# Performance work log

Measured on AMD Instinct MI355X. Metric: run time of the kernel, lower is better.

The kernel has to match this reference:

```python
import jax, jax.numpy as jnp
import numpy as np

HEADS = 8
D = 1024


def setup_inputs() -> dict:
    key = jax.random.key(0)
    ks = jax.random.split(key, 10)
    B, Sq, Sk = 8, 2048, 2048
    x = jax.random.normal(ks[0], (B, Sq, D), dtype=jnp.float32)
    context = jax.random.normal(ks[1], (B, Sk, D), dtype=jnp.float32)
    # Dense params (glorot-ish scale)
    def dense(k, fin, fout):
        return jax.random.normal(k, (fin, fout), dtype=jnp.float32) / np.sqrt(fin)
    Wq = dense(ks[2], D, HEADS); bq = jnp.zeros((HEADS,), jnp.float32)
    Wk = dense(ks[3], D, HEADS); bk = jnp.zeros((HEADS,), jnp.float32)
    Wv = dense(ks[4], D, HEADS); bv = jnp.zeros((HEADS,), jnp.float32)
    Wo = dense(ks[5], HEADS, D); bo = jnp.zeros((D,), jnp.float32)
    return {"x": x, "context": context, "Wq": Wq, "bq": bq,
            "Wk": Wk, "bk": bk, "Wv": Wv, "bv": bv, "Wo": Wo, "bo": bo}


def reference(x, context, Wq, bq, Wk, bk, Wv, bv, Wo, bo):
    # q: [B,Sq,H], k/v: [B,Sk,H]  (H = heads = projection width, no head split)
    q = jnp.einsum('bsd,dh->bsh', x, Wq) + bq
    k = jnp.einsum('btd,dh->bth', context, Wk) + bk
    v = jnp.einsum('btd,dh->bth', context, Wv) + bv
    # Dot(axes=-1): scores[b,s,t] = q[b,s,:] . k[b,t,:]  -> [B,Sq,Sk]
    scores = jnp.einsum('bsh,bth->bst', q, k)
    weights = jax.nn.softmax(scores, axis=-1)  # no 1/sqrt(d) scaling in original
    # Dot(axes=(-1,1)): out[b,s,h] = sum_t weights[b,s,t] * v[b,t,h]
    out = jnp.einsum('bst,bth->bsh', weights, v)
    return jnp.einsum('bsh,hd->bsd', out, Wo) + bo
```

## Files before the change

kernel.cpp:

```cpp
#include <hip/hip_runtime.h>

constexpr int D = 1024;
constexpr int H = 8;
constexpr int S = 2048;
constexpr int B = 8;
constexpr int NROW = B * S;

__global__ __launch_bounds__(256)
void proj_kernel(const float* __restrict__ x, const float* __restrict__ ctx,
                 const float* __restrict__ Wq, const float* __restrict__ bq,
                 const float* __restrict__ Wk, const float* __restrict__ bk,
                 const float* __restrict__ Wv, const float* __restrict__ bv,
                 float* __restrict__ qo, float* __restrict__ ko,
                 float* __restrict__ vo)
{
    __shared__ float4 xt[32 * 64];
    __shared__ float  red[4 * 64 * 8];

    const int tid   = threadIdx.x;
    const int lane  = tid & 63;
    const int wid_v = tid >> 6;
    const int wid   = __builtin_amdgcn_readfirstlane(wid_v);

    const int bid = (int)blockIdx.x;
    const int tensor = (bid >> 3) % 3;
    const int blk    = (bid / 24) * 8 + (bid & 7);

    const float* W    = (tensor == 0) ? Wq : (tensor == 1) ? Wk : Wv;
    const float* bias = (tensor == 0) ? bq : (tensor == 1) ? bk : bv;
    const float* src  = (tensor == 0) ? x  : ctx;
    float*       dst  = (tensor == 0) ? qo : (tensor == 1) ? ko : vo;

    const int row0 = blk * 64;
    const float4* x4 = (const float4*)src + (size_t)row0 * 256;

    float acc[8];
#pragma unroll
    for (int h = 0; h < 8; ++h) acc[h] = 0.f;

    const int sk4    = tid & 31;
    const int srow_b = tid >> 5;
    const float4* gsrc = x4 + (size_t)srow_b * 256 + sk4;
    const int wbase = sk4 * 64 + (srow_b ^ (sk4 & 7));

    float4 f0 = gsrc[0 * 2048], f1 = gsrc[1 * 2048],
           f2 = gsrc[2 * 2048], f3 = gsrc[3 * 2048],
           f4 = gsrc[4 * 2048], f5 = gsrc[5 * 2048],
           f6 = gsrc[6 * 2048], f7 = gsrc[7 * 2048];

    for (int chunk = 0; chunk < 8; ++chunk) {
        xt[wbase + 0 * 8] = f0;  xt[wbase + 1 * 8] = f1;
        xt[wbase + 2 * 8] = f2;  xt[wbase + 3 * 8] = f3;
        xt[wbase + 4 * 8] = f4;  xt[wbase + 5 * 8] = f5;
        xt[wbase + 6 * 8] = f6;  xt[wbase + 7 * 8] = f7;
        __syncthreads();

        if (chunk < 7) {
            const int o = (chunk + 1) * 32;
            f0 = gsrc[0 * 2048 + o];  f1 = gsrc[1 * 2048 + o];
            f2 = gsrc[2 * 2048 + o];  f3 = gsrc[3 * 2048 + o];
            f4 = gsrc[4 * 2048 + o];  f5 = gsrc[5 * 2048 + o];
            f6 = gsrc[6 * 2048 + o];  f7 = gsrc[7 * 2048 + o];
        }

#pragma unroll 4
        for (int i = 0; i < 8; ++i) {
            const int k4 = wid * 8 + i;
            const float4 xv = xt[k4 * 64 + (lane ^ (k4 & 7))];
            const float* Wb = W + ((size_t)chunk * 128 + k4 * 4) * 8;
#pragma unroll
            for (int e = 0; e < 4; ++e) {
                const float xs = (&xv.x)[e];
                acc[0] += xs * Wb[e * 8 + 0];
                acc[1] += xs * Wb[e * 8 + 1];
                acc[2] += xs * Wb[e * 8 + 2];
                acc[3] += xs * Wb[e * 8 + 3];
                acc[4] += xs * Wb[e * 8 + 4];
                acc[5] += xs * Wb[e * 8 + 5];
                acc[6] += xs * Wb[e * 8 + 6];
                acc[7] += xs * Wb[e * 8 + 7];
            }
        }
        __syncthreads();
    }

    float4* red4 = (float4*)red;
    red4[wid_v * 128 + lane * 2 + 0] = make_float4(acc[0], acc[1], acc[2], acc[3]);
    red4[wid_v * 128 + lane * 2 + 1] = make_float4(acc[4], acc[5], acc[6], acc[7]);
    __syncthreads();

    const int oi   = tid * 2;
    const int orow = oi >> 3;
    const int oh   = oi & 7;
    float s0 = bias[oh], s1 = bias[oh + 1];
#pragma unroll
    for (int w = 0; w < 4; ++w) {
        s0 += red[w * 512 + orow * 8 + oh];
        s1 += red[w * 512 + orow * 8 + oh + 1];
    }
    *(float2*)(dst + (size_t)(row0 + orow) * H + oh) = make_float2(s0, s1);
}

constexpr int RPW = 4;
constexpr int RPB = 16;
constexpr int TILE_T = 512;

__global__ __launch_bounds__(256)
void attn_kernel(const float* __restrict__ q, const float* __restrict__ k,
                 const float* __restrict__ v, const float* __restrict__ Wo,
                 const float* __restrict__ bo, float* __restrict__ out)
{
    __shared__ float4 ka[TILE_T], kb[TILE_T];
    __shared__ float4 va[TILE_T], vb[TILE_T];
    const int tid  = threadIdx.x;
    const int lane = tid & 63;
    const int wid  = tid >> 6;

    const int row0 = blockIdx.x * RPB + wid * RPW;
    const int b = row0 >> 11;

    float qv[RPW][H];
#pragma unroll
    for (int r = 0; r < RPW; ++r) {
        const float4* q4 = (const float4*)(q + (size_t)(row0 + r) * H);
        const float4 a = q4[0], c = q4[1];
        qv[r][0] = a.x; qv[r][1] = a.y; qv[r][2] = a.z; qv[r][3] = a.w;
        qv[r][4] = c.x; qv[r][5] = c.y; qv[r][6] = c.z; qv[r][7] = c.w;
    }

    float l[RPW] = {0.f, 0.f, 0.f, 0.f};
    float o[RPW][H];
#pragma unroll
    for (int r = 0; r < RPW; ++r)
#pragma unroll
        for (int h = 0; h < H; ++h) o[r][h] = 0.f;

    const float4* kg = (const float4*)(k + (size_t)b * S * H);
    const float4* vg = (const float4*)(v + (size_t)b * S * H);

    for (int tile = 0; tile < S / TILE_T; ++tile) {
        __syncthreads();
#pragma unroll
        for (int i = 0; i < TILE_T / 256; ++i) {
            const int t = i * 256 + tid;
            const int g = tile * TILE_T + t;
            ka[t] = kg[2 * g];  kb[t] = kg[2 * g + 1];
            va[t] = vg[2 * g];  vb[t] = vg[2 * g + 1];
        }
        __syncthreads();

        float4 k0 = ka[lane], k1 = kb[lane];
        float4 v0 = va[lane], v1 = vb[lane];
#pragma unroll
        for (int m = 0; m < TILE_T / 64; ++m) {
            float4 nk0, nk1, nv0, nv1;
            if (m + 1 < TILE_T / 64) {
                const int t = lane + ((m + 1) << 6);
                nk0 = ka[t]; nk1 = kb[t]; nv0 = va[t]; nv1 = vb[t];
            }
#pragma unroll
            for (int r = 0; r < RPW; ++r) {
                const float s = qv[r][0] * k0.x + qv[r][1] * k0.y
                              + qv[r][2] * k0.z + qv[r][3] * k0.w
                              + qv[r][4] * k1.x + qv[r][5] * k1.y
                              + qv[r][6] * k1.z + qv[r][7] * k1.w;
                const float e = __expf(s);
                l[r] += e;
                o[r][0] += e * v0.x; o[r][1] += e * v0.y;
                o[r][2] += e * v0.z; o[r][3] += e * v0.w;
                o[r][4] += e * v1.x; o[r][5] += e * v1.y;
                o[r][6] += e * v1.z; o[r][7] += e * v1.w;
            }
            if (m + 1 < TILE_T / 64) {
                k0 = nk0; k1 = nk1; v0 = nv0; v1 = nv1;
            }
        }
    }

#pragma unroll
    for (int r = 0; r < RPW; ++r) {
#pragma unroll
        for (int off = 32; off > 0; off >>= 1) l[r] += __shfl_xor(l[r], off);
        const float inv = 1.f / l[r];
#pragma unroll
        for (int h = 0; h < H; ++h) {
#pragma unroll
            for (int off = 32; off > 0; off >>= 1) o[r][h] += __shfl_xor(o[r][h], off);
            o[r][h] *= inv;
        }
    }

    const float4* Wo4 = (const float4*)Wo;
    const float4* bo4 = (const float4*)bo;
    float4* out4 = (float4*)out;
#pragma unroll
    for (int c = 0; c < 4; ++c) {
        const int f = lane + 64 * c;
        float4 w[H];
#pragma unroll
        for (int h = 0; h < H; ++h) w[h] = Wo4[h * (D / 4) + f];
        const float4 base = bo4[f];
#pragma unroll
        for (int r = 0; r < RPW; ++r) {
            float4 acc = base;
#pragma unroll
            for (int h = 0; h < H; ++h) {
                acc.x += o[r][h] * w[h].x;
                acc.y += o[r][h] * w[h].y;
                acc.z += o[r][h] * w[h].z;
                acc.w += o[r][h] * w[h].w;
            }
            out4[(size_t)(row0 + r) * (D / 4) + f] = acc;
        }
    }
}

extern "C" void kernel_launch(void* const* d_in, const int* in_sizes, int n_in,
                              void* d_out, int out_size, void* d_ws, size_t ws_size,
                              hipStream_t stream) {
    const float* x   = (const float*)d_in[0];
    const float* ctx = (const float*)d_in[1];
    const float* Wq  = (const float*)d_in[2];
    const float* bq  = (const float*)d_in[3];
    const float* Wk  = (const float*)d_in[4];
    const float* bk  = (const float*)d_in[5];
    const float* Wv  = (const float*)d_in[6];
    const float* bv  = (const float*)d_in[7];
    const float* Wo  = (const float*)d_in[8];
    const float* bo  = (const float*)d_in[9];
    float* out = (float*)d_out;

    float* qw = (float*)d_ws;
    float* kw = qw + (size_t)NROW * H;
    float* vw = kw + (size_t)NROW * H;

    proj_kernel<<<dim3(3 * NROW / 64), dim3(256), 0, stream>>>(
        x, ctx, Wq, bq, Wk, bk, Wv, bv, qw, kw, vw);
    attn_kernel<<<dim3(NROW / RPB), dim3(256), 0, stream>>>(
        qw, kw, vw, Wo, bo, out);
}
```

Baseline: 222.8 us.

## Deepen projection prefetch to two chunks and read K/V directly from global in attention

The projection kernel now keeps two register buffers of input data in flight, issuing global loads two chunks ahead so load latency overlaps more compute. The attention kernel drops its shared-memory K/V tiles and block-wide barriers. Each wave instead streams K/V straight from global memory with a one-step register prefetch, relying on L1/L2 caching because all waves in a block read the same data. This removes LDS traffic and syncs at the cost of more register pressure and repeated global or cache reads per wave.

```diff
diff --git a/kernel.cpp b/kernel.cpp
--- a/kernel.cpp
+++ b/kernel.cpp
@@ -43,26 +43,7 @@
     const float4* gsrc = x4 + (size_t)srow_b * 256 + sk4;
     const int wbase = sk4 * 64 + (srow_b ^ (sk4 & 7));
 
-    float4 f0 = gsrc[0 * 2048], f1 = gsrc[1 * 2048],
-           f2 = gsrc[2 * 2048], f3 = gsrc[3 * 2048],
-           f4 = gsrc[4 * 2048], f5 = gsrc[5 * 2048],
-           f6 = gsrc[6 * 2048], f7 = gsrc[7 * 2048];
-
-    for (int chunk = 0; chunk < 8; ++chunk) {
-        xt[wbase + 0 * 8] = f0;  xt[wbase + 1 * 8] = f1;
-        xt[wbase + 2 * 8] = f2;  xt[wbase + 3 * 8] = f3;
-        xt[wbase + 4 * 8] = f4;  xt[wbase + 5 * 8] = f5;
-        xt[wbase + 6 * 8] = f6;  xt[wbase + 7 * 8] = f7;
-        __syncthreads();
-
-        if (chunk < 7) {
-            const int o = (chunk + 1) * 32;
-            f0 = gsrc[0 * 2048 + o];  f1 = gsrc[1 * 2048 + o];
-            f2 = gsrc[2 * 2048 + o];  f3 = gsrc[3 * 2048 + o];
-            f4 = gsrc[4 * 2048 + o];  f5 = gsrc[5 * 2048 + o];
-            f6 = gsrc[6 * 2048 + o];  f7 = gsrc[7 * 2048 + o];
-        }
-
+    auto compute = [&](int chunk) {
 #pragma unroll 4
         for (int i = 0; i < 8; ++i) {
             const int k4 = wid * 8 + i;
@@ -81,6 +62,46 @@
                 acc[7] += xs * Wb[e * 8 + 7];
             }
         }
+    };
+
+    float4 f0 = gsrc[0 * 2048 +  0], f1 = gsrc[1 * 2048 +  0],
+           f2 = gsrc[2 * 2048 +  0], f3 = gsrc[3 * 2048 +  0],
+           f4 = gsrc[4 * 2048 +  0], f5 = gsrc[5 * 2048 +  0],
+           f6 = gsrc[6 * 2048 +  0], f7 = gsrc[7 * 2048 +  0];
+    float4 g0 = gsrc[0 * 2048 + 32], g1 = gsrc[1 * 2048 + 32],
+           g2 = gsrc[2 * 2048 + 32], g3 = gsrc[3 * 2048 + 32],
+           g4 = gsrc[4 * 2048 + 32], g5 = gsrc[5 * 2048 + 32],
+           g6 = gsrc[6 * 2048 + 32], g7 = gsrc[7 * 2048 + 32];
+
+    for (int c = 0; c < 8; c += 2) {
+        xt[wbase + 0 * 8] = f0;  xt[wbase + 1 * 8] = f1;
+        xt[wbase + 2 * 8] = f2;  xt[wbase + 3 * 8] = f3;
+        xt[wbase + 4 * 8] = f4;  xt[wbase + 5 * 8] = f5;
+        xt[wbase + 6 * 8] = f6;  xt[wbase + 7 * 8] = f7;
+        __syncthreads();
+        if (c + 2 < 8) {
+            const int o = (c + 2) * 32;
+            f0 = gsrc[0 * 2048 + o];  f1 = gsrc[1 * 2048 + o];
+            f2 = gsrc[2 * 2048 + o];  f3 = gsrc[3 * 2048 + o];
+            f4 = gsrc[4 * 2048 + o];  f5 = gsrc[5 * 2048 + o];
+            f6 = gsrc[6 * 2048 + o];  f7 = gsrc[7 * 2048 + o];
+        }
+        compute(c);
+        __syncthreads();
+
+        xt[wbase + 0 * 8] = g0;  xt[wbase + 1 * 8] = g1;
+        xt[wbase + 2 * 8] = g2;  xt[wbase + 3 * 8] = g3;
+        xt[wbase + 4 * 8] = g4;  xt[wbase + 5 * 8] = g5;
+        xt[wbase + 6 * 8] = g6;  xt[wbase + 7 * 8] = g7;
+        __syncthreads();
+        if (c + 3 < 8) {
+            const int o = (c + 3) * 32;
+            g0 = gsrc[0 * 2048 + o];  g1 = gsrc[1 * 2048 + o];
+            g2 = gsrc[2 * 2048 + o];  g3 = gsrc[3 * 2048 + o];
+            g4 = gsrc[4 * 2048 + o];  g5 = gsrc[5 * 2048 + o];
+            g6 = gsrc[6 * 2048 + o];  g7 = gsrc[7 * 2048 + o];
+        }
+        compute(c + 1);
         __syncthreads();
     }
 
@@ -103,15 +124,12 @@
 
 constexpr int RPW = 4;
 constexpr int RPB = 16;
-constexpr int TILE_T = 512;
 
 __global__ __launch_bounds__(256)
 void attn_kernel(const float* __restrict__ q, const float* __restrict__ k,
                  const float* __restrict__ v, const float* __restrict__ Wo,
                  const float* __restrict__ bo, float* __restrict__ out)
 {
-    __shared__ float4 ka[TILE_T], kb[TILE_T];
-    __shared__ float4 va[TILE_T], vb[TILE_T];
     const int tid  = threadIdx.x;
     const int lane = tid & 63;
     const int wid  = tid >> 6;
@@ -138,42 +156,30 @@
     const float4* kg = (const float4*)(k + (size_t)b * S * H);
     const float4* vg = (const float4*)(v + (size_t)b * S * H);
 
-    for (int tile = 0; tile < S / TILE_T; ++tile) {
-        __syncthreads();
-#pragma unroll
-        for (int i = 0; i < TILE_T / 256; ++i) {
-            const int t = i * 256 + tid;
-            const int g = tile * TILE_T + t;
-            ka[t] = kg[2 * g];  kb[t] = kg[2 * g + 1];
-            va[t] = vg[2 * g];  vb[t] = vg[2 * g + 1];
-        }
-        __syncthreads();
-
-        float4 k0 = ka[lane], k1 = kb[lane];
-        float4 v0 = va[lane], v1 = vb[lane];
-#pragma unroll
-        for (int m = 0; m < TILE_T / 64; ++m) {
-            float4 nk0, nk1, nv0, nv1;
-            if (m + 1 < TILE_T / 64) {
-                const int t = lane + ((m + 1) << 6);
-                nk0 = ka[t]; nk1 = kb[t]; nv0 = va[t]; nv1 = vb[t];
-            }
-#pragma unroll
-            for (int r = 0; r < RPW; ++r) {
-                const float s = qv[r][0] * k0.x + qv[r][1] * k0.y
-                              + qv[r][2] * k0.z + qv[r][3] * k0.w
-                              + qv[r][4] * k1.x + qv[r][5] * k1.y
-                              + qv[r][6] * k1.z + qv[r][7] * k1.w;
-                const float e = __expf(s);
-                l[r] += e;
-                o[r][0] += e * v0.x; o[r][1] += e * v0.y;
-                o[r][2] += e * v0.z; o[r][3] += e * v0.w;
-                o[r][4] += e * v1.x; o[r][5] += e * v1.y;
-                o[r][6] += e * v1.z; o[r][7] += e * v1.w;
-            }
-            if (m + 1 < TILE_T / 64) {
-                k0 = nk0; k1 = nk1; v0 = nv0; v1 = nv1;
-            }
+    float4 k0 = kg[lane * 2], k1 = kg[lane * 2 + 1];
+    float4 v0 = vg[lane * 2], v1 = vg[lane * 2 + 1];
+#pragma unroll 2
+    for (int m = 0; m < S / 64; ++m) {
+        float4 nk0, nk1, nv0, nv1;
+        if (m + 1 < S / 64) {
+            const int t2 = (lane + ((m + 1) << 6)) * 2;
+            nk0 = kg[t2]; nk1 = kg[t2 + 1]; nv0 = vg[t2]; nv1 = vg[t2 + 1];
+        }
+#pragma unroll
+        for (int r = 0; r < RPW; ++r) {
+            const float s = qv[r][0] * k0.x + qv[r][1] * k0.y
+                          + qv[r][2] * k0.z + qv[r][3] * k0.w
+                          + qv[r][4] * k1.x + qv[r][5] * k1.y
+                          + qv[r][6] * k1.z + qv[r][7] * k1.w;
+            const float e = __expf(s);
+            l[r] += e;
+            o[r][0] += e * v0.x; o[r][1] += e * v0.y;
+            o[r][2] += e * v0.z; o[r][3] += e * v0.w;
+            o[r][4] += e * v1.x; o[r][5] += e * v1.y;
+            o[r][6] += e * v1.z; o[r][7] += e * v1.w;
+        }
+        if (m + 1 < S / 64) {
+            k0 = nk0; k1 = nk1; v0 = nv0; v1 = nv1;
         }
     }
 
```

Result: slower. 234.4 us (+5.2%).
